# Optimization experiments

Hardware: AMD Instinct MI355X
Metric: run time of the kernel (lower is better)

## Reference

```python
import jax, jax.numpy as jnp
import numpy as np

B, T, IN_DIM, UNITS, PEAK_DIM = 64, 1024, 256, 512, 512


def setup_inputs() -> dict:
    key = jax.random.key(0)
    ks = jax.random.split(key, 6)
    s = lambda fan: 1.0 / np.sqrt(fan)
    return {
        "x": jax.random.normal(ks[0], (B, T, IN_DIM), dtype=jnp.float32),
        "peak": jax.random.normal(ks[1], (B, PEAK_DIM), dtype=jnp.float32),
        "kernel": jax.random.normal(ks[2], (IN_DIM, 3 * UNITS), dtype=jnp.float32) * s(IN_DIM),
        "recurrent_kernel": jax.random.normal(ks[3], (UNITS, 3 * UNITS), dtype=jnp.float32) * s(UNITS),
        "peak_kernel": jax.random.normal(ks[4], (PEAK_DIM, 3 * UNITS), dtype=jnp.float32) * s(PEAK_DIM),
        "bias": jnp.zeros((3 * UNITS,), dtype=jnp.float32),
        "peak_initial": jax.random.normal(ks[5], (PEAK_DIM, UNITS), dtype=jnp.float32) * s(PEAK_DIM),
    }


def _hard_sigmoid(a):
    # Keras hard_sigmoid: clip(0.2*x + 0.5, 0, 1)
    return jnp.clip(0.2 * a + 0.5, 0.0, 1.0)


def reference(x, peak, kernel, recurrent_kernel, peak_kernel, bias, peak_initial):
    U = peak_initial.shape[1]
    # Initial state from peak context: h0 = peak @ peak_initial  [B, U]
    h0 = jnp.dot(peak, peak_initial)
    # Precompute time-invariant projections (same math as per-step dots).
    xp = jnp.einsum("bti,ik->btk", x, kernel) + bias          # [B, T, 3U]
    pp = jnp.dot(peak, peak_kernel)                              # [B, 3U]

    def step(h, xt):
        hp = jnp.dot(h, recurrent_kernel)                        # [B, 3U]
        zr = _hard_sigmoid(xt[:, : 2 * U] + hp[:, : 2 * U] + pp[:, : 2 * U])
        z, r = zr[:, :U], zr[:, U:]
        hh = jnp.tanh(xt[:, 2 * U :] + r * (hp[:, 2 * U :] + pp[:, 2 * U :]))
        h_new = z * h + (1.0 - z) * hh
        return h_new, h_new

    xs = jnp.swapaxes(xp, 0, 1)                                  # [T, B, 3U]
    _, hs = jax.lax.scan(step, h0, xs)                           # [T, B, U]
    return jnp.swapaxes(hs, 0, 1)                                # [B, T, U]
```

## Files before the change

kernel.cpp:

```cpp
#include <hip/hip_runtime.h>
#include <hip/hip_bf16.h>

#define B_   64
#define T_   1024
#define IND_ 256
#define U_   512
#define G3_  1536
#define BPG   8
#define SLOTS 32

typedef unsigned int u32;
typedef unsigned short u16;
typedef unsigned long long u64;
typedef __attribute__((ext_vector_type(8))) short short8;
typedef __attribute__((ext_vector_type(4))) float f32x4;
typedef __attribute__((ext_vector_type(4))) unsigned int u32x4;

union S8 { short8 v; u16 us[8]; u32 d[4]; u64 q[2]; };
union BF { __hip_bfloat16 b; u16 u; };

__device__ __forceinline__ u16 f2b(float f){ BF t; t.b = __float2bfloat16(f); return t.u; }
__device__ __forceinline__ float hsig(float a){ return fminf(fmaxf(fmaf(a, 0.2f, 0.5f), 0.f), 1.f); }
__device__ __forceinline__ u32 umax2(u32 a, u32 b){ return a > b ? a : b; }
__device__ __forceinline__ float fast_tanh(float x){
  float ax = fabsf(x);
  float e  = __expf(ax + ax);
  float r  = 1.f - 2.f / (e + 1.f);
  return copysignf(r, x);
}
__device__ __forceinline__ void drain_vm(){
  asm volatile("s_waitcnt vmcnt(0)" ::: "memory");
  __builtin_amdgcn_sched_barrier(0);
}
__device__ __forceinline__ void st_sys(u32* p, u32 v){
  asm volatile("global_store_dword %0, %1, off sc0 sc1" :: "v"(p), "v"(v) : "memory");
}
__device__ __forceinline__ u32 ld_sys(const u32* p){
  u32 v;
  asm volatile("global_load_dword %0, %1, off sc0 sc1\n\ts_waitcnt vmcnt(0)"
               : "=v"(v) : "v"(p) : "memory");
  return v;
}
__device__ __forceinline__ void st16_sys(u32* p, u32x4 v){
  asm volatile("global_store_dwordx4 %0, %1, off sc0 sc1" :: "v"(p), "v"(v) : "memory");
}

#define LDA16(aa, hb) \
  asm volatile( \
    "global_load_dwordx4 %0,  %16, off sc0 sc1\n\t" \
    "global_load_dwordx4 %1,  %16, off offset:64 sc0 sc1\n\t" \
    "global_load_dwordx4 %2,  %16, off offset:128 sc0 sc1\n\t" \
    "global_load_dwordx4 %3,  %16, off offset:192 sc0 sc1\n\t" \
    "global_load_dwordx4 %4,  %16, off offset:256 sc0 sc1\n\t" \
    "global_load_dwordx4 %5,  %16, off offset:320 sc0 sc1\n\t" \
    "global_load_dwordx4 %6,  %16, off offset:384 sc0 sc1\n\t" \
    "global_load_dwordx4 %7,  %16, off offset:448 sc0 sc1\n\t" \
    "global_load_dwordx4 %8,  %16, off offset:512 sc0 sc1\n\t" \
    "global_load_dwordx4 %9,  %16, off offset:576 sc0 sc1\n\t" \
    "global_load_dwordx4 %10, %16, off offset:640 sc0 sc1\n\t" \
    "global_load_dwordx4 %11, %16, off offset:704 sc0 sc1\n\t" \
    "global_load_dwordx4 %12, %16, off offset:768 sc0 sc1\n\t" \
    "global_load_dwordx4 %13, %16, off offset:832 sc0 sc1\n\t" \
    "global_load_dwordx4 %14, %16, off offset:896 sc0 sc1\n\t" \
    "global_load_dwordx4 %15, %16, off offset:960 sc0 sc1\n\t" \
    "s_waitcnt vmcnt(0)" \
    : "=&v"(aa[0].v),  "=&v"(aa[1].v),  "=&v"(aa[2].v),  "=&v"(aa[3].v), \
      "=&v"(aa[4].v),  "=&v"(aa[5].v),  "=&v"(aa[6].v),  "=&v"(aa[7].v), \
      "=&v"(aa[8].v),  "=&v"(aa[9].v),  "=&v"(aa[10].v), "=&v"(aa[11].v), \
      "=&v"(aa[12].v), "=&v"(aa[13].v), "=&v"(aa[14].v), "=&v"(aa[15].v) \
    : "v"(hb) : "memory")


__global__ void k_zero(u32* c) {
  int i = threadIdx.x;
  for (int k = i; k < 1024; k += 256) c[k] = 0u;
}

__global__ void k_fill(u32x4* p) {
  size_t i = (size_t)blockIdx.x * 256 + threadIdx.x;
  u32x4 v = {0xFFFFFFFFu, 0xFFFFFFFFu, 0xFFFFFFFFu, 0xFFFFFFFFu};
  p[i] = v;
}

__global__ void k_wt(const float* __restrict__ rk, const float* __restrict__ xk,
                     u16* __restrict__ WrT, u16* __restrict__ WxT) {
  int i = blockIdx.x * 256 + threadIdx.x;
  if (i < U_ * G3_) {
    int k = i / G3_, c = i - k * G3_;
    WrT[(size_t)c * U_ + k] = f2b(rk[i]);
  } else {
    int j = i - U_ * G3_;
    int k = j / G3_, c = j - k * G3_;
    WxT[(size_t)c * IND_ + k] = f2b(xk[j]);
  }
}

__global__ void k_xb(const float* __restrict__ x, u16* __restrict__ xb) {
  size_t i = ((size_t)blockIdx.x * 256 + threadIdx.x) * 8;
  const float4* p = (const float4*)(x + i);
  float4 a = p[0], b = p[1];
  S8 o;
  o.us[0]=f2b(a.x); o.us[1]=f2b(a.y); o.us[2]=f2b(a.z); o.us[3]=f2b(a.w);
  o.us[4]=f2b(b.x); o.us[5]=f2b(b.y); o.us[6]=f2b(b.z); o.us[7]=f2b(b.w);
  *(short8*)(xb + i) = o.v;
}

__global__ void k_pp(const float* __restrict__ peak, const float* __restrict__ pk,
                     float* __restrict__ pp) {
  int i = blockIdx.x * 256 + threadIdx.x;
  int b = i / G3_, c = i - b * G3_;
  const float* pr = peak + b * U_;
  float s = 0.f;
  for (int k = 0; k < U_; ++k) s = fmaf(pr[k], pk[(size_t)k * G3_ + c], s);
  pp[i] = s;
}

__global__ void k_h0(const float* __restrict__ peak, const float* __restrict__ pi,
                     float* __restrict__ h0, u16* __restrict__ hb0) {
  int i = blockIdx.x * 256 + threadIdx.x;
  int b = i >> 9, u = i & 511;
  const float* pr = peak + b * U_;
  float s = 0.f;
  for (int k = 0; k < U_; ++k) s = fmaf(pr[k], pi[(size_t)k * U_ + u], s);
  h0[i] = s;
  if (hb0) hb0[i] = f2b(s);
}


template<bool XBQ>
__global__ __launch_bounds__(64, 1) void k_scan_s(
    const void* __restrict__ xsrc, const float* __restrict__ bias,
    const float* __restrict__ pp, const float* __restrict__ h0,
    const u16* __restrict__ WrT, const u16* __restrict__ WxT,
    u16* __restrict__ hbuf, float* __restrict__ out)
{
  __shared__ short8 lB[4608];

  const int tid = threadIdx.x;
  const int g = blockIdx.x & 3;
  const int s = blockIdx.x >> 2;
  const int scol0 = s * 16;

  for (int lin = tid; lin < 3072; lin += 64) {
    int lp = lin & 63, ks = (lin >> 6) & 15, gate = lin >> 10;
    int cc = lp & 15, kk = lp >> 4;
    lB[lin] = *(const short8*)(WrT + (size_t)(gate * U_ + scol0 + cc) * U_ + ks * 32 + kk * 8);
  }
  for (int lin = tid; lin < 1536; lin += 64) {
    int lp = lin & 63, ks = (lin >> 6) & 7, gate = lin >> 9;
    int cc = lp & 15, kk = lp >> 4;
    lB[3072 + lin] = *(const short8*)(WxT + (size_t)(gate * U_ + scol0 + cc) * IND_ + ks * 32 + kk * 8);
  }
  __syncthreads();

  const int c   = tid & 15;
  const int kg  = tid >> 4;
  const int col = scol0 + c;

  float bpz[4], bpr[4], pph[4], hprev[4];
  float bh = bias[2 * U_ + col];
#pragma unroll
  for (int q = 0; q < 4; ++q) {
    int bg = g * 16 + kg * 4 + q;
    bpz[q]   = bias[col]       + pp[(size_t)bg * G3_ + col];
    bpr[q]   = bias[U_ + col]  + pp[(size_t)bg * G3_ + U_ + col];
    pph[q]   = pp[(size_t)bg * G3_ + 2 * U_ + col];
    hprev[q] = h0[(size_t)bg * U_ + col];
  }

  const u16*   xbrow = (const u16*)xsrc   + (size_t)(g * 16 + c) * T_ * IND_;
  const float* xfrow = (const float*)xsrc + (size_t)(g * 16 + c) * T_ * IND_;
  const f32x4 z4 = {0.f, 0.f, 0.f, 0.f};
  f32x4 pxz = z4, pxr = z4, pxh = z4;
  S8 xa[8];

#define XMFMA(AZ, AR, AH) do { \
    _Pragma("unroll") \
    for (int ks = 0; ks < 8; ++ks) { \
      AZ = __builtin_amdgcn_mfma_f32_16x16x32_bf16(xa[ks].v, lB[3072 + (0*8+ks)*64 + tid], AZ, 0,0,0); \
      AR = __builtin_amdgcn_mfma_f32_16x16x32_bf16(xa[ks].v, lB[3072 + (1*8+ks)*64 + tid], AR, 0,0,0); \
      AH = __builtin_amdgcn_mfma_f32_16x16x32_bf16(xa[ks].v, lB[3072 + (2*8+ks)*64 + tid], AH, 0,0,0); \
    } \
  } while (0)
#define XLOAD(tt) do { \
    if constexpr (XBQ) { \
      _Pragma("unroll") \
      for (int ks = 0; ks < 8; ++ks) \
        xa[ks].v = *(const short8*)(xbrow + (size_t)(tt) * IND_ + kg * 8 + ks * 32); \
    } else { \
      _Pragma("unroll") \
      for (int ks = 0; ks < 8; ++ks) { \
        const float4* p4_ = (const float4*)(xfrow + (size_t)(tt) * IND_ + kg * 8 + ks * 32); \
        float4 x0_ = p4_[0], x1_ = p4_[1]; \
        xa[ks].us[0]=f2b(x0_.x); xa[ks].us[1]=f2b(x0_.y); xa[ks].us[2]=f2b(x0_.z); xa[ks].us[3]=f2b(x0_.w); \
        xa[ks].us[4]=f2b(x1_.x); xa[ks].us[5]=f2b(x1_.y); xa[ks].us[6]=f2b(x1_.z); xa[ks].us[7]=f2b(x1_.w); \
      } \
    } \
  } while (0)

  XLOAD(0);
  XMFMA(pxz, pxr, pxh);

  for (int t = 0; t < T_; ++t) {
    const u16* hb = hbuf + (size_t)t * (B_ * U_) + (size_t)(g * 16 + c) * U_ + kg * 8;
    S8 aa[16];
    for (;;) {
      LDA16(aa, hb);
      u32 mx = 0;
#pragma unroll
      for (int ks = 0; ks < 16; ++ks)
        mx = umax2(mx, umax2(umax2(aa[ks].d[0], aa[ks].d[1]),
                             umax2(aa[ks].d[2], aa[ks].d[3])));
      if (__all((int)(mx < 0xFFFF0000u))) break;
    }

    if (t < T_ - 1) XLOAD(t + 1);

    f32x4 az = pxz, ar = pxr, ah = pxh, ahr = z4;
#pragma unroll
    for (int ks = 0; ks < 16; ++ks) {
      az  = __builtin_amdgcn_mfma_f32_16x16x32_bf16(aa[ks].v, lB[(0*16+ks)*64 + tid], az,  0,0,0);
      ar  = __builtin_amdgcn_mfma_f32_16x16x32_bf16(aa[ks].v, lB[(1*16+ks)*64 + tid], ar,  0,0,0);
      ahr = __builtin_amdgcn_mfma_f32_16x16x32_bf16(aa[ks].v, lB[(2*16+ks)*64 + tid], ahr, 0,0,0);
    }

    float hnew[4];
#pragma unroll
    for (int q = 0; q < 4; ++q) {
      float z  = hsig(az[q] + bpz[q]);
      float r  = hsig(ar[q] + bpr[q]);
      float hh = fast_tanh(ah[q] + bh + r * (ahr[q] + pph[q]));
      hnew[q] = fmaf(z, hprev[q] - hh, hh);
      hprev[q] = hnew[q];
    }

    u16* hb1 = hbuf + (size_t)(t + 1) * (B_ * U_);
#pragma unroll
    for (int q = 0; q < 4; ++q) {
      u32 hv = (u32)f2b(hnew[q]);
      u32 w0 = hv | ((u32)__shfl_xor((int)hv, 1) << 16);
      u32 w1 = (u32)__shfl_xor((int)w0, 2);
      u32 w2 = (u32)__shfl_xor((int)w0, 4);
      u32 w3 = (u32)__shfl_xor((int)w1, 4);
      if (!(c & 7)) {
        u32x4 vv = {w0, w1, w2, w3};
        st16_sys((u32*)(hb1 + (size_t)(g * 16 + kg * 4 + q) * U_ + scol0 + c), vv);
      }
    }

#pragma unroll
    for (int q = 0; q < 4; ++q) {
      int bg = g * 16 + kg * 4 + q;
      out[((size_t)bg * T_ + t) * U_ + col] = hnew[q];
    }
    if (t < T_ - 1) {
      pxz = z4; pxr = z4; pxh = z4;
      XMFMA(pxz, pxr, pxh);
    }
  }
#undef XMFMA
#undef XLOAD
}


template<bool XBQ>
__global__ __launch_bounds__(64, 1) void k_scan_fb(
    const void* __restrict__ xsrc, const float* __restrict__ bias,
    const float* __restrict__ pp, const float* __restrict__ h0,
    const u16* __restrict__ WrT, const u16* __restrict__ WxT,
    u16* __restrict__ hbuf, u32* __restrict__ cnt, float* __restrict__ out)
{
  __shared__ short8 lB[4608];

  const int tid = threadIdx.x;
  const int g = blockIdx.x & 7;
  const int s = blockIdx.x >> 3;
  const int scol0 = s * 16;

  for (int lin = tid; lin < 3072; lin += 64) {
    int lp = lin & 63, ks = (lin >> 6) & 15, gate = lin >> 10;
    int cc = lp & 15, kk = lp >> 4;
    lB[lin] = *(const short8*)(WrT + (size_t)(gate * U_ + scol0 + cc) * U_ + ks * 32 + kk * 8);
  }
  for (int lin = tid; lin < 1536; lin += 64) {
    int lp = lin & 63, ks = (lin >> 6) & 7, gate = lin >> 9;
    int cc = lp & 15, kk = lp >> 4;
    lB[3072 + lin] = *(const short8*)(WxT + (size_t)(gate * U_ + scol0 + cc) * IND_ + ks * 32 + kk * 8);
  }
  __syncthreads();

  const int c   = tid & 15;
  const int kg  = tid >> 4;
  const int col = scol0 + c;
  const int kge = kg & 1;

  float bpz[4], bpr[4], pph[4], hprev[4];
  float bh = bias[2 * U_ + col];
#pragma unroll
  for (int q = 0; q < 4; ++q) {
    int bg = g * BPG + kge * 4 + q;
    bpz[q]   = bias[col]       + pp[(size_t)bg * G3_ + col];
    bpr[q]   = bias[U_ + col]  + pp[(size_t)bg * G3_ + U_ + col];
    pph[q]   = pp[(size_t)bg * G3_ + 2 * U_ + col];
    hprev[q] = h0[(size_t)bg * U_ + col];
  }

  u16* hbA = hbuf + (size_t)(g * 2 + 0) * BPG * U_;
  u16* hbB = hbuf + (size_t)(g * 2 + 1) * BPG * U_;
  u32* cntp  = cnt + g * 32;
  u32* flags = cnt + 256 + g * 64;
  const u32* fp = flags + (tid & 31);

#pragma unroll
  for (int q = 0; q < 4; ++q) {
    u32 hv = (u32)f2b(hprev[q]);
    u32 ov = (u32)__shfl_xor((int)hv, 1);
    if (kg < 2 && !(c & 1))
      __hip_atomic_store((u32*)(hbA + (size_t)(kg * 4 + q) * U_ + col), hv | (ov << 16),
                         __ATOMIC_RELAXED, __HIP_MEMORY_SCOPE_AGENT);
  }
  drain_vm();
  if (tid == 0)
    __hip_atomic_fetch_add(cntp, 1u, __ATOMIC_RELAXED, __HIP_MEMORY_SCOPE_AGENT);

  const u16*   xbrow = (const u16*)xsrc   + (size_t)(g * BPG + (c & 7)) * T_ * IND_;
  const float* xfrow = (const float*)xsrc + (size_t)(g * BPG + (c & 7)) * T_ * IND_;
  const f32x4 z4 = {0.f, 0.f, 0.f, 0.f};
  f32x4 pxz = z4, pxr = z4, pxh = z4;

#define GEMM_XFB(tt, AZ, AR, AH) do { \
    _Pragma("unroll") \
    for (int ks = 0; ks < 8; ++ks) { \
      S8 a_; \
      if constexpr (XBQ) { \
        a_.v = *(const short8*)(xbrow + (size_t)(tt) * IND_ + kg * 8 + ks * 32); \
      } else { \
        const float4* p4_ = (const float4*)(xfrow + (size_t)(tt) * IND_ + kg * 8 + ks * 32); \
        float4 x0_ = p4_[0], x1_ = p4_[1]; \
        a_.us[0]=f2b(x0_.x); a_.us[1]=f2b(x0_.y); a_.us[2]=f2b(x0_.z); a_.us[3]=f2b(x0_.w); \
        a_.us[4]=f2b(x1_.x); a_.us[5]=f2b(x1_.y); a_.us[6]=f2b(x1_.z); a_.us[7]=f2b(x1_.w); \
      } \
      AZ = __builtin_amdgcn_mfma_f32_16x16x32_bf16(a_.v, lB[3072 + (0*8+ks)*64 + tid], AZ, 0,0,0); \
      AR = __builtin_amdgcn_mfma_f32_16x16x32_bf16(a_.v, lB[3072 + (1*8+ks)*64 + tid], AR, 0,0,0); \
      AH = __builtin_amdgcn_mfma_f32_16x16x32_bf16(a_.v, lB[3072 + (2*8+ks)*64 + tid], AH, 0,0,0); \
    } \
  } while (0)

  GEMM_XFB(0, pxz, pxr, pxh);

  while (__hip_atomic_load(cntp, __ATOMIC_RELAXED, __HIP_MEMORY_SCOPE_AGENT) < (u32)SLOTS)
    __builtin_amdgcn_s_sleep(1);

  for (int t = 0; t < T_; ++t) {
    const u16* hb = ((t & 1) ? hbB : hbA) + (size_t)(c & 7) * U_ + kg * 8;
    S8 aa[16];
    LDA16(aa, hb);

    f32x4 az = pxz, ar = pxr, ah = pxh, ahr = z4;
#pragma unroll
    for (int ks = 0; ks < 16; ++ks) {
      az  = __builtin_amdgcn_mfma_f32_16x16x32_bf16(aa[ks].v, lB[(0*16+ks)*64 + tid], az,  0,0,0);
      ar  = __builtin_amdgcn_mfma_f32_16x16x32_bf16(aa[ks].v, lB[(1*16+ks)*64 + tid], ar,  0,0,0);
      ahr = __builtin_amdgcn_mfma_f32_16x16x32_bf16(aa[ks].v, lB[(2*16+ks)*64 + tid], ahr, 0,0,0);
    }

    float hnew[4];
#pragma unroll
    for (int q = 0; q < 4; ++q) {
      float z  = hsig(az[q] + bpz[q]);
      float r  = hsig(ar[q] + bpr[q]);
      float hh = fast_tanh(ah[q] + bh + r * (ahr[q] + pph[q]));
      hnew[q] = fmaf(z, hprev[q] - hh, hh);
      hprev[q] = hnew[q];
    }

    u16* ho = (t & 1) ? hbA : hbB;
#pragma unroll
    for (int q = 0; q < 4; ++q) {
      u32 hv = (u32)f2b(hnew[q]);
      u32 ov = (u32)__shfl_xor((int)hv, 1);
      if (kg < 2 && !(c & 1))
        __hip_atomic_store((u32*)(ho + (size_t)(kg * 4 + q) * U_ + col), hv | (ov << 16),
                           __ATOMIC_RELAXED, __HIP_MEMORY_SCOPE_AGENT);
    }
    drain_vm();
    if (tid == 0) st_sys((u32*)(flags + s), (u32)(t + 1));

    if (t < T_ - 1) {
      pxz = z4; pxr = z4; pxh = z4;
      GEMM_XFB(t + 1, pxz, pxr, pxh);
    }
    if (kg < 2) {
#pragma unroll
      for (int q = 0; q < 4; ++q) {
        int bg = g * BPG + kg * 4 + q;
        out[((size_t)bg * T_ + t) * U_ + col] = hnew[q];
      }
    }
    if (t < T_ - 1) {
      u32 target = (u32)(t + 1);
      while (true) {
        u32 v = ld_sys(fp);
        if (__all((int)(v >= target))) break;
        __builtin_amdgcn_s_sleep(1);
      }
    }
  }
#undef GEMM_XFB
}


extern "C" void kernel_launch(void* const* d_in, const int* in_sizes, int n_in,
                              void* d_out, int out_size, void* d_ws, size_t ws_size,
                              hipStream_t stream) {
  const float* x    = (const float*)d_in[0];
  const float* peak = (const float*)d_in[1];
  const float* xk   = (const float*)d_in[2];
  const float* rk   = (const float*)d_in[3];
  const float* pk   = (const float*)d_in[4];
  const float* pi   = (const float*)d_in[6];
  const float* bias = (const float*)d_in[5];
  float* out = (float*)d_out;

  char* w = (char*)d_ws;
  u16*   WrT = (u16*)(w);
  u16*   WxT = (u16*)(w + 1572864);
  float* pp  = (float*)(w + 2359296);
  float* h0  = (float*)(w + 2752512);

  const size_t HBUF_BYTES = (size_t)(T_ + 1) * B_ * U_ * 2;
  const size_t NEED_S_XB  = (size_t)36438016 + HBUF_BYTES;
  const size_t NEED_S_F32 = (size_t)2883584  + HBUF_BYTES;
  const size_t NEED_FB_XB = (size_t)36573184;

  k_wt<<<dim3(4608), dim3(256), 0, stream>>>(rk, xk, WrT, WxT);
  k_pp<<<dim3(384),  dim3(256), 0, stream>>>(peak, pk, pp);

  if (ws_size >= NEED_S_XB) {
    u16* xb   = (u16*)(w + 2883584);
    u16* hbuf = (u16*)(w + 36438016);
    k_fill<<<dim3((unsigned)(HBUF_BYTES / 16 / 256)), dim3(256), 0, stream>>>((u32x4*)hbuf);
    k_h0  <<<dim3(128),  dim3(256), 0, stream>>>(peak, pi, h0, hbuf);
    k_xb  <<<dim3(8192), dim3(256), 0, stream>>>(x, xb);
    k_scan_s<true><<<dim3(128), dim3(64), 0, stream>>>(xb, bias, pp, h0, WrT, WxT, hbuf, out);
  } else if (ws_size >= NEED_S_F32) {
    u16* hbuf = (u16*)(w + 2883584);
    k_fill<<<dim3((unsigned)(HBUF_BYTES / 16 / 256)), dim3(256), 0, stream>>>((u32x4*)hbuf);
    k_h0  <<<dim3(128), dim3(256), 0, stream>>>(peak, pi, h0, hbuf);
    k_scan_s<false><<<dim3(128), dim3(64), 0, stream>>>(x, bias, pp, h0, WrT, WxT, hbuf, out);
  } else {
    u16* hbuf = (u16*)(w + 2883584);
    u32* cnt  = (u32*)(w + 3014656);
    k_zero<<<dim3(1),   dim3(256), 0, stream>>>(cnt);
    k_h0  <<<dim3(128), dim3(256), 0, stream>>>(peak, pi, h0, (u16*)nullptr);
    if (ws_size >= NEED_FB_XB) {
      u16* xb = (u16*)(w + 3018752);
      k_xb<<<dim3(8192), dim3(256), 0, stream>>>(x, xb);
      k_scan_fb<true><<<dim3(256), dim3(64), 0, stream>>>(xb, bias, pp, h0, WrT, WxT, hbuf, cnt, out);
    } else {
      k_scan_fb<false><<<dim3(256), dim3(64), 0, stream>>>(x, bias, pp, h0, WrT, WxT, hbuf, cnt, out);
    }
  }
}
```

Baseline: 3.179 ms.

## Overlap hidden-state polling with next-step input projection, batch output stores

Restructures the persistent GRU scan loop. It issues the hidden-state loads first, computes the next step's input-projection MFMAs while those loads are in flight, and only then waits and polls. It also double-buffers the x fragments two steps ahead, replaces shuffle-packed 16-byte system stores with 4-byte paired stores, and unrolls by four so the output writes are buffered and sent as nontemporal stores. The aim is to hide global-memory latency on the serial critical path, at the cost of more registers and more, smaller coherent stores.

```diff
diff --git a/kernel.cpp b/kernel.cpp
--- a/kernel.cpp
+++ b/kernel.cpp
@@ -41,9 +41,30 @@
                : "=v"(v) : "v"(p) : "memory");
   return v;
 }
-__device__ __forceinline__ void st16_sys(u32* p, u32x4 v){
-  asm volatile("global_store_dwordx4 %0, %1, off sc0 sc1" :: "v"(p), "v"(v) : "memory");
-}
+
+#define LDA16_ISSUE(aa, hb) \
+  asm volatile( \
+    "global_load_dwordx4 %0,  %16, off sc0 sc1\n\t" \
+    "global_load_dwordx4 %1,  %16, off offset:64 sc0 sc1\n\t" \
+    "global_load_dwordx4 %2,  %16, off offset:128 sc0 sc1\n\t" \
+    "global_load_dwordx4 %3,  %16, off offset:192 sc0 sc1\n\t" \
+    "global_load_dwordx4 %4,  %16, off offset:256 sc0 sc1\n\t" \
+    "global_load_dwordx4 %5,  %16, off offset:320 sc0 sc1\n\t" \
+    "global_load_dwordx4 %6,  %16, off offset:384 sc0 sc1\n\t" \
+    "global_load_dwordx4 %7,  %16, off offset:448 sc0 sc1\n\t" \
+    "global_load_dwordx4 %8,  %16, off offset:512 sc0 sc1\n\t" \
+    "global_load_dwordx4 %9,  %16, off offset:576 sc0 sc1\n\t" \
+    "global_load_dwordx4 %10, %16, off offset:640 sc0 sc1\n\t" \
+    "global_load_dwordx4 %11, %16, off offset:704 sc0 sc1\n\t" \
+    "global_load_dwordx4 %12, %16, off offset:768 sc0 sc1\n\t" \
+    "global_load_dwordx4 %13, %16, off offset:832 sc0 sc1\n\t" \
+    "global_load_dwordx4 %14, %16, off offset:896 sc0 sc1\n\t" \
+    "global_load_dwordx4 %15, %16, off offset:960 sc0 sc1" \
+    : "=&v"(aa[0].v),  "=&v"(aa[1].v),  "=&v"(aa[2].v),  "=&v"(aa[3].v), \
+      "=&v"(aa[4].v),  "=&v"(aa[5].v),  "=&v"(aa[6].v),  "=&v"(aa[7].v), \
+      "=&v"(aa[8].v),  "=&v"(aa[9].v),  "=&v"(aa[10].v), "=&v"(aa[11].v), \
+      "=&v"(aa[12].v), "=&v"(aa[13].v), "=&v"(aa[14].v), "=&v"(aa[15].v) \
+    : "v"(hb) : "memory")
 
 #define LDA16(aa, hb) \
   asm volatile( \
@@ -171,93 +192,98 @@
   const u16*   xbrow = (const u16*)xsrc   + (size_t)(g * 16 + c) * T_ * IND_;
   const float* xfrow = (const float*)xsrc + (size_t)(g * 16 + c) * T_ * IND_;
   const f32x4 z4 = {0.f, 0.f, 0.f, 0.f};
-  f32x4 pxz = z4, pxr = z4, pxh = z4;
-  S8 xa[8];
-
-#define XMFMA(AZ, AR, AH) do { \
-    _Pragma("unroll") \
-    for (int ks = 0; ks < 8; ++ks) { \
-      AZ = __builtin_amdgcn_mfma_f32_16x16x32_bf16(xa[ks].v, lB[3072 + (0*8+ks)*64 + tid], AZ, 0,0,0); \
-      AR = __builtin_amdgcn_mfma_f32_16x16x32_bf16(xa[ks].v, lB[3072 + (1*8+ks)*64 + tid], AR, 0,0,0); \
-      AH = __builtin_amdgcn_mfma_f32_16x16x32_bf16(xa[ks].v, lB[3072 + (2*8+ks)*64 + tid], AH, 0,0,0); \
-    } \
-  } while (0)
-#define XLOAD(tt) do { \
+  S8 xaA[8], xaB[8];
+  f32x4 pxzA, pxrA, pxhA, pxzB, pxrB, pxhB;
+  float ob[4][4];
+
+#define XLOAD(tt, XA) do { \
     if constexpr (XBQ) { \
       _Pragma("unroll") \
       for (int ks = 0; ks < 8; ++ks) \
-        xa[ks].v = *(const short8*)(xbrow + (size_t)(tt) * IND_ + kg * 8 + ks * 32); \
+        XA[ks].v = *(const short8*)(xbrow + (size_t)(tt) * IND_ + kg * 8 + ks * 32); \
     } else { \
       _Pragma("unroll") \
       for (int ks = 0; ks < 8; ++ks) { \
         const float4* p4_ = (const float4*)(xfrow + (size_t)(tt) * IND_ + kg * 8 + ks * 32); \
         float4 x0_ = p4_[0], x1_ = p4_[1]; \
-        xa[ks].us[0]=f2b(x0_.x); xa[ks].us[1]=f2b(x0_.y); xa[ks].us[2]=f2b(x0_.z); xa[ks].us[3]=f2b(x0_.w); \
-        xa[ks].us[4]=f2b(x1_.x); xa[ks].us[5]=f2b(x1_.y); xa[ks].us[6]=f2b(x1_.z); xa[ks].us[7]=f2b(x1_.w); \
+        XA[ks].us[0]=f2b(x0_.x); XA[ks].us[1]=f2b(x0_.y); XA[ks].us[2]=f2b(x0_.z); XA[ks].us[3]=f2b(x0_.w); \
+        XA[ks].us[4]=f2b(x1_.x); XA[ks].us[5]=f2b(x1_.y); XA[ks].us[6]=f2b(x1_.z); XA[ks].us[7]=f2b(x1_.w); \
       } \
     } \
   } while (0)
 
-  XLOAD(0);
-  XMFMA(pxz, pxr, pxh);
-
-  for (int t = 0; t < T_; ++t) {
-    const u16* hb = hbuf + (size_t)t * (B_ * U_) + (size_t)(g * 16 + c) * U_ + kg * 8;
-    S8 aa[16];
-    for (;;) {
-      LDA16(aa, hb);
-      u32 mx = 0;
-#pragma unroll
-      for (int ks = 0; ks < 16; ++ks)
-        mx = umax2(mx, umax2(umax2(aa[ks].d[0], aa[ks].d[1]),
-                             umax2(aa[ks].d[2], aa[ks].d[3])));
-      if (__all((int)(mx < 0xFFFF0000u))) break;
-    }
-
-    if (t < T_ - 1) XLOAD(t + 1);
-
-    f32x4 az = pxz, ar = pxr, ah = pxh, ahr = z4;
-#pragma unroll
-    for (int ks = 0; ks < 16; ++ks) {
-      az  = __builtin_amdgcn_mfma_f32_16x16x32_bf16(aa[ks].v, lB[(0*16+ks)*64 + tid], az,  0,0,0);
-      ar  = __builtin_amdgcn_mfma_f32_16x16x32_bf16(aa[ks].v, lB[(1*16+ks)*64 + tid], ar,  0,0,0);
-      ahr = __builtin_amdgcn_mfma_f32_16x16x32_bf16(aa[ks].v, lB[(2*16+ks)*64 + tid], ahr, 0,0,0);
-    }
-
-    float hnew[4];
-#pragma unroll
-    for (int q = 0; q < 4; ++q) {
-      float z  = hsig(az[q] + bpz[q]);
-      float r  = hsig(ar[q] + bpr[q]);
-      float hh = fast_tanh(ah[q] + bh + r * (ahr[q] + pph[q]));
-      hnew[q] = fmaf(z, hprev[q] - hh, hh);
-      hprev[q] = hnew[q];
-    }
-
-    u16* hb1 = hbuf + (size_t)(t + 1) * (B_ * U_);
-#pragma unroll
-    for (int q = 0; q < 4; ++q) {
-      u32 hv = (u32)f2b(hnew[q]);
-      u32 w0 = hv | ((u32)__shfl_xor((int)hv, 1) << 16);
-      u32 w1 = (u32)__shfl_xor((int)w0, 2);
-      u32 w2 = (u32)__shfl_xor((int)w0, 4);
-      u32 w3 = (u32)__shfl_xor((int)w1, 4);
-      if (!(c & 7)) {
-        u32x4 vv = {w0, w1, w2, w3};
-        st16_sys((u32*)(hb1 + (size_t)(g * 16 + kg * 4 + q) * U_ + scol0 + c), vv);
+#define XMFMA(XA, AZ, AR, AH) do { \
+    _Pragma("unroll") \
+    for (int ks = 0; ks < 8; ++ks) { \
+      AZ = __builtin_amdgcn_mfma_f32_16x16x32_bf16(XA[ks].v, lB[3072 + (0*8+ks)*64 + tid], AZ, 0,0,0); \
+      AR = __builtin_amdgcn_mfma_f32_16x16x32_bf16(XA[ks].v, lB[3072 + (1*8+ks)*64 + tid], AR, 0,0,0); \
+      AH = __builtin_amdgcn_mfma_f32_16x16x32_bf16(XA[ks].v, lB[3072 + (2*8+ks)*64 + tid], AH, 0,0,0); \
+    } \
+  } while (0)
+
+  XLOAD(0, xaB);
+  pxzA = z4; pxrA = z4; pxhA = z4;
+  XMFMA(xaB, pxzA, pxrA, pxhA);
+  XLOAD(1, xaA);
+
+#define STEP(J, XAC, XAN, PXZC, PXRC, PXHC, PXZN, PXRN, PXHN) do { \
+    const int t = tb + (J); \
+    const u16* hb = hbuf + (size_t)t * (B_ * U_) + (size_t)(g * 16 + c) * U_ + kg * 8; \
+    S8 aa[16]; \
+    LDA16_ISSUE(aa, hb); \
+    PXZN = z4; PXRN = z4; PXHN = z4; \
+    if (t < T_ - 1) XMFMA(XAC, PXZN, PXRN, PXHN);    \
+    __builtin_amdgcn_sched_barrier(0); \
+    asm volatile("s_waitcnt vmcnt(0)" ::: "memory"); \
+    __builtin_amdgcn_sched_barrier(0); \
+    for (;;) { \
+      u32 mx = 0; \
+      _Pragma("unroll") \
+      for (int ks = 0; ks < 16; ++ks) \
+        mx = umax2(mx, umax2(umax2(aa[ks].d[0], aa[ks].d[1]), \
+                             umax2(aa[ks].d[2], aa[ks].d[3]))); \
+      if (__all((int)(mx < 0xFFFF0000u))) break; \
+      LDA16(aa, hb); \
+    } \
+    if (t < T_ - 2) XLOAD(t + 2, XAN);               \
+    f32x4 az = PXZC, ar = PXRC, ah = PXHC, ahr = z4; \
+    _Pragma("unroll") \
+    for (int ks = 0; ks < 16; ++ks) { \
+      az  = __builtin_amdgcn_mfma_f32_16x16x32_bf16(aa[ks].v, lB[(0*16+ks)*64 + tid], az,  0,0,0); \
+      ar  = __builtin_amdgcn_mfma_f32_16x16x32_bf16(aa[ks].v, lB[(1*16+ks)*64 + tid], ar,  0,0,0); \
+      ahr = __builtin_amdgcn_mfma_f32_16x16x32_bf16(aa[ks].v, lB[(2*16+ks)*64 + tid], ahr, 0,0,0); \
+    } \
+    u16* hb1 = hbuf + (size_t)(t + 1) * (B_ * U_); \
+    _Pragma("unroll") \
+    for (int q = 0; q < 4; ++q) { \
+      float z  = hsig(az[q] + bpz[q]); \
+      float r  = hsig(ar[q] + bpr[q]); \
+      float hh = fast_tanh(ah[q] + bh + r * (ahr[q] + pph[q])); \
+      float hn = fmaf(z, hprev[q] - hh, hh); \
+      hprev[q] = hn; \
+      ob[J][q] = hn; \
+      u32 hv = (u32)f2b(hn); \
+      u32 ov = (u32)__shfl_xor((int)hv, 1); \
+      if (!(c & 1)) \
+        st_sys((u32*)(hb1 + (size_t)(g * 16 + kg * 4 + q) * U_ + scol0 + c), hv | (ov << 16)); \
+    } \
+  } while (0)
+
+  for (int tb = 0; tb < T_; tb += 4) {
+    STEP(0, xaA, xaB, pxzA, pxrA, pxhA, pxzB, pxrB, pxhB);
+    STEP(1, xaB, xaA, pxzB, pxrB, pxhB, pxzA, pxrA, pxhA);
+    STEP(2, xaA, xaB, pxzA, pxrA, pxhA, pxzB, pxrB, pxhB);
+    STEP(3, xaB, xaA, pxzB, pxrB, pxhB, pxzA, pxrA, pxhA);
+#pragma unroll
+    for (int j = 0; j < 4; ++j) {
+#pragma unroll
+      for (int q = 0; q < 4; ++q) {
+        int bg = g * 16 + kg * 4 + q;
+        __builtin_nontemporal_store(ob[j][q], out + ((size_t)bg * T_ + (tb + j)) * U_ + col);
       }
     }
-
-#pragma unroll
-    for (int q = 0; q < 4; ++q) {
-      int bg = g * 16 + kg * 4 + q;
-      out[((size_t)bg * T_ + t) * U_ + col] = hnew[q];
-    }
-    if (t < T_ - 1) {
-      pxz = z4; pxr = z4; pxh = z4;
-      XMFMA(pxz, pxr, pxh);
-    }
-  }
+  }
+#undef STEP
 #undef XMFMA
 #undef XLOAD
 }
@@ -418,8 +444,8 @@
   const float* xk   = (const float*)d_in[2];
   const float* rk   = (const float*)d_in[3];
   const float* pk   = (const float*)d_in[4];
+  const float* bias = (const float*)d_in[5];
   const float* pi   = (const float*)d_in[6];
-  const float* bias = (const float*)d_in[5];
   float* out = (float*)d_out;
 
   char* w = (char*)d_ws;
```

After: 4.247 ms. +33.6%, slower.
